# Kernel optimization log

Hardware: AMD Instinct MI355X
Metric: run time of the kernel (lower is better)

## Reference

```python
import jax, jax.numpy as jnp
import numpy as np

SENSORS = 50000
X_DIM = 64
HID = 64
Y_DIM = 32
N_EDGES = 800000


def setup_inputs() -> dict:
    key = jax.random.key(0)
    k0, k1, k2, k3 = jax.random.split(key, 4)
    x_input = jax.random.normal(k0, (1, X_DIM, SENSORS), dtype=jnp.float32)
    edge_index = jax.random.randint(k1, (2, N_EDGES), 0, SENSORS, dtype=jnp.int32)
    # GCNConv parameters (glorot-ish scaling)
    W1 = jax.random.normal(k2, (X_DIM, HID), dtype=jnp.float32) / np.sqrt(X_DIM)
    b1 = jnp.zeros((HID,), dtype=jnp.float32)
    W2 = jax.random.normal(k3, (HID, Y_DIM), dtype=jnp.float32) / np.sqrt(HID)
    b2 = jnp.zeros((Y_DIM,), dtype=jnp.float32)
    return {"x_input": x_input, "W1": W1, "b1": b1, "W2": W2, "b2": b2,
            "edge_index": edge_index}


def _gcn_conv(x, W, b, src, dst, n_nodes):
    """PyG GCNConv: x' = D^{-1/2}(A+I)D^{-1/2} (x W) + b."""
    h = x @ W  # [N, F_out]
    loop = jnp.arange(n_nodes, dtype=src.dtype)
    s = jnp.concatenate([src, loop])  # add self-loops
    d = jnp.concatenate([dst, loop])
    deg = jax.ops.segment_sum(jnp.ones_like(d, dtype=h.dtype), d,
                              num_segments=n_nodes)
    dinv = jnp.where(deg > 0, jax.lax.rsqrt(deg), 0.0)
    norm = dinv[s] * dinv[d]  # [E+N]
    msg = h[s] * norm[:, None]  # gather source features, scale
    out = jax.ops.segment_sum(msg, d, num_segments=n_nodes)  # scatter-add to targets
    return out + b


def reference(x_input, W1, b1, W2, b2, edge_index):
    B = x_input.shape[0]
    # [B, x, S] -> [B, S, x] -> [B*S, x]
    h = jnp.transpose(x_input, (0, 2, 1)).reshape(-1, X_DIM)
    n_nodes = h.shape[0]
    src, dst = edge_index[0], edge_index[1]
    h = _gcn_conv(h, W1, b1, src, dst, n_nodes)
    h = jax.nn.relu(h)
    h = _gcn_conv(h, W2, b2, src, dst, n_nodes)
    # [B*S, y] -> [B, S, y] -> [B, y, S]
    return jnp.transpose(h.reshape(B, SENSORS, Y_DIM), (0, 2, 1))
```

## Files before the change

### kernel.cpp

```cpp
#include <hip/hip_runtime.h>

#define NS 50000
#define NE 800000
#define XD 64
#define HD 64
#define YD 32

#define SHIFT 7
#define BNODES 128
#define NBUCK 391
#define BCAP 2560
#define NBLKA 256
#define EPB (NE / NBLKA)
#define SCAP 32
#define XW_BLKS ((NS + 255) / 256)

__device__ __forceinline__ unsigned f2b(float f) {
    union { float f; unsigned u; } c; c.f = f;
    return (c.u + 0x7fffu + ((c.u >> 16) & 1u)) >> 16;
}
__device__ __forceinline__ float blo(unsigned u) {
    union { unsigned u; float f; } c; c.u = u << 16; return c.f;
}
__device__ __forceinline__ float bhi(unsigned u) {
    union { unsigned u; float f; } c; c.u = u & 0xffff0000u; return c.f;
}

__global__ __launch_bounds__(256) void k_bktxw1(const int* __restrict__ src,
                                                const int* __restrict__ dst,
                                                int* __restrict__ cnt2,
                                                unsigned* __restrict__ ebuf2,
                                                const float* __restrict__ x,
                                                const float* __restrict__ W1,
                                                unsigned* __restrict__ G1h) {
    __shared__ unsigned se[EPB];
    __shared__ unsigned short lp[EPB];
    __shared__ int hist[NBUCK];
    __shared__ float w1f[XD * HD];
    int t = threadIdx.x;
    if (blockIdx.x < NBLKA) {
        int blk = blockIdx.x;
        int lo = blk * EPB;
        for (int i = t; i < NBUCK; i += 256) hist[i] = 0;
        __syncthreads();
        for (int i = t; i < EPB; i += 256) {
            unsigned d = (unsigned)__builtin_nontemporal_load(dst + lo + i);
            unsigned s = (unsigned)__builtin_nontemporal_load(src + lo + i);
            se[i] = (d << 16) | s;
            lp[i] = (unsigned short)atomicAdd(&hist[d >> SHIFT], 1);
        }
        __syncthreads();
        for (int i = t; i < NBUCK; i += 256)
            cnt2[blk * NBUCK + i] = min(hist[i], SCAP);
        for (int i = t; i < EPB; i += 256) {
            unsigned p = se[i];
            int b = p >> (16 + SHIFT);
            int pos = lp[i];
            if (pos < SCAP)
                ebuf2[((size_t)b * NBLKA + blk) * SCAP + pos] = p;
        }
        return;
    }
    for (int i = t; i < XD * HD; i += 256) w1f[i] = W1[i];
    __syncthreads();
    int node = (blockIdx.x - NBLKA) * 256 + t;
    if (node >= NS) return;
    float4 acc[16];
#pragma unroll
    for (int i = 0; i < 16; ++i) acc[i] = make_float4(0.f, 0.f, 0.f, 0.f);
    for (int xf = 0; xf < XD; ++xf) {
        float xv = __builtin_nontemporal_load(&x[(size_t)xf * NS + node]);
        const float4* wr = (const float4*)&w1f[xf * HD];
#pragma unroll
        for (int i = 0; i < 16; ++i) {
            float4 wv = wr[i];
            acc[i].x += xv * wv.x; acc[i].y += xv * wv.y;
            acc[i].z += xv * wv.z; acc[i].w += xv * wv.w;
        }
    }
    unsigned pk[32];
#pragma unroll
    for (int i = 0; i < 16; ++i) {
        pk[2 * i]     = f2b(acc[i].x) | (f2b(acc[i].y) << 16);
        pk[2 * i + 1] = f2b(acc[i].z) | (f2b(acc[i].w) << 16);
    }
    uint4* o = (uint4*)&G1h[(size_t)node * 32];
#pragma unroll
    for (int i = 0; i < 8; ++i) o[i] = ((uint4*)pk)[i];
}

__global__ __launch_bounds__(256) void k_sort(const unsigned* __restrict__ ebuf2,
                                              const int* __restrict__ cnt2,
                                              unsigned short* __restrict__ csr,
                                              int* __restrict__ beg,
                                              int* __restrict__ endp,
                                              float* __restrict__ dinv,
                                              unsigned* __restrict__ G1h) {
    __shared__ unsigned se[BCAP];
    __shared__ unsigned short lcsr[BCAP];
    __shared__ int cnt[BNODES];
    __shared__ int offl[BNODES];
    __shared__ int cur[BNODES];
    __shared__ int sm[256];
    __shared__ int wsum[4];
    int b = blockIdx.x, t = threadIdx.x;
    int lane = t & 63, w = t >> 6;
    int c = cnt2[t * NBUCK + b];
    int v = c;
#pragma unroll
    for (int d = 1; d < 64; d <<= 1) {
        int o = __shfl_up(v, d);
        if (lane >= d) v += o;
    }
    if (lane == 63) wsum[w] = v;
    if (t < BNODES) cnt[t] = 0;
    __syncthreads();
    int wpre = 0;
#pragma unroll
    for (int i = 0; i < 4; ++i) wpre += (i < w) ? wsum[i] : 0;
    int soff = wpre + v - c;
    int ntot = wsum[0] + wsum[1] + wsum[2] + wsum[3];
    int n = min(ntot, BCAP);
    {
        const unsigned* sb = ebuf2 + ((size_t)b * NBLKA + t) * SCAP;
        for (int j = 0; j < c; j += 4) {
            uint4 vv = *(const uint4*)&sb[j];
            int p = soff + j;
            if (p < BCAP) se[p] = vv.x;
            if (j + 1 < c && p + 1 < BCAP) se[p + 1] = vv.y;
            if (j + 2 < c && p + 2 < BCAP) se[p + 2] = vv.z;
            if (j + 3 < c && p + 3 < BCAP) se[p + 3] = vv.w;
        }
    }
    __syncthreads();
    for (int i = t; i < n; i += 256) atomicAdd(&cnt[(se[i] >> 16) & (BNODES - 1)], 1);
    __syncthreads();
    int v2 = (t < BNODES) ? cnt[t] : 0;
    sm[t] = v2;
    __syncthreads();
    int val2 = v2;
    for (int o = 1; o < BNODES; o <<= 1) {
        int other = (t >= o) ? sm[t - o] : 0;
        __syncthreads();
        val2 += other;
        sm[t] = val2;
        __syncthreads();
    }
    if (t < BNODES) { offl[t] = val2 - v2; cur[t] = val2 - v2; }
    __syncthreads();
    for (int i = t; i < n; i += 256) {
        unsigned p = se[i];
        int l = (p >> 16) & (BNODES - 1);
        int pos = atomicAdd(&cur[l], 1);
        lcsr[pos] = (unsigned short)(p & 0xffffu);
    }
    __syncthreads();
    unsigned* gc = (unsigned*)(csr + (size_t)b * BCAP);
    int nw = (n + 1) >> 1;
    for (int i = t; i < nw; i += 256) gc[i] = ((const unsigned*)lcsr)[i];
    if (t < BNODES) {
        int node = b * BNODES + t;
        if (node < NS) {
            int bg = b * BCAP + offl[t];
            beg[node] = bg;
            endp[node] = bg + cnt[t];
            dinv[node] = rsqrtf((float)cnt[t] + 1.0f);
        }
    }
    int tn = t >> 1, hf = t & 1;
    int node = b * BNODES + tn;
    if (node >= NS) return;
    float dv = rsqrtf((float)cnt[tn] + 1.0f);
    uint4* row = (uint4*)&G1h[(size_t)node * 32 + hf * 16];
#pragma unroll
    for (int i = 0; i < 4; ++i) {
        uint4 u = row[i];
        u.x = f2b(dv * blo(u.x)) | (f2b(dv * bhi(u.x)) << 16);
        u.y = f2b(dv * blo(u.y)) | (f2b(dv * bhi(u.y)) << 16);
        u.z = f2b(dv * blo(u.z)) | (f2b(dv * bhi(u.z)) << 16);
        u.w = f2b(dv * blo(u.w)) | (f2b(dv * bhi(u.w)) << 16);
        row[i] = u;
    }
}

__global__ __launch_bounds__(256) void k_g1l2(const int* __restrict__ beg,
                                              const int* __restrict__ endp,
                                              const unsigned short* __restrict__ csr,
                                              const unsigned* __restrict__ G1h,
                                              const float* __restrict__ dinv,
                                              const float* __restrict__ b1,
                                              const float* __restrict__ W2,
                                              unsigned* __restrict__ G2h) {
    __shared__ float w2s[HD * YD];
    __shared__ float bsh[HD];
    __shared__ float lds_h[16][68];
    __shared__ float lds_dv[16];
    int t = threadIdx.x;
    for (int i = t; i < HD * YD; i += 256) w2s[i] = W2[i];
    if (t < HD) bsh[t] = b1[t];
    __syncthreads();

    int nl = t >> 4;
    int l  = t & 15;
    int node = blockIdx.x * 16 + nl;
    int beg_ = beg[node], end_ = endp[node];
    float a0 = 0.f, a1 = 0.f, a2 = 0.f, a3 = 0.f;
#pragma unroll 4
    for (int e = beg_; e < end_; ++e) {
        int s = (int)csr[e];
        uint2 u = *(const uint2*)&G1h[(unsigned)s * 32u + 2u * l];
        a0 += blo(u.x); a1 += bhi(u.x);
        a2 += blo(u.y); a3 += bhi(u.y);
    }
    uint2 us = *(const uint2*)&G1h[(unsigned)node * 32u + 2u * l];
    float dv = dinv[node];
    float4 h;
    h.x = fmaxf(fmaf(dv, a0 + blo(us.x), bsh[4 * l + 0]), 0.f);
    h.y = fmaxf(fmaf(dv, a1 + bhi(us.x), bsh[4 * l + 1]), 0.f);
    h.z = fmaxf(fmaf(dv, a2 + blo(us.y), bsh[4 * l + 2]), 0.f);
    h.w = fmaxf(fmaf(dv, a3 + bhi(us.y), bsh[4 * l + 3]), 0.f);
    *(float4*)&lds_h[nl][4 * l] = h;
    if (l == 0) lds_dv[nl] = dv;
    __syncthreads();

    int n2 = t >> 4;
    int oo = (t & 15) * 2;
    float dv2 = lds_dv[n2];
    const float* hr = &lds_h[n2][0];
    float p0 = 0.f, p1 = 0.f;
#pragma unroll
    for (int f4 = 0; f4 < 16; ++f4) {
        float4 hv = *(const float4*)&hr[f4 * 4];
        float2 wa = *(const float2*)&w2s[(f4 * 4 + 0) * YD + oo];
        float2 wb = *(const float2*)&w2s[(f4 * 4 + 1) * YD + oo];
        float2 wc = *(const float2*)&w2s[(f4 * 4 + 2) * YD + oo];
        float2 wd = *(const float2*)&w2s[(f4 * 4 + 3) * YD + oo];
        p0 = fmaf(hv.x, wa.x, p0); p1 = fmaf(hv.x, wa.y, p1);
        p0 = fmaf(hv.y, wb.x, p0); p1 = fmaf(hv.y, wb.y, p1);
        p0 = fmaf(hv.z, wc.x, p0); p1 = fmaf(hv.z, wc.y, p1);
        p0 = fmaf(hv.w, wd.x, p0); p1 = fmaf(hv.w, wd.y, p1);
    }
    int node2 = blockIdx.x * 16 + n2;
    G2h[(size_t)node2 * 16 + (t & 15)] = f2b(dv2 * p0) | (f2b(dv2 * p1) << 16);
}

__global__ __launch_bounds__(256) void k_g2out(const int* __restrict__ beg,
                                               const int* __restrict__ endp,
                                               const unsigned short* __restrict__ csr,
                                               const unsigned* __restrict__ G2h,
                                               const float* __restrict__ dinv,
                                               const float* __restrict__ b2,
                                               float* __restrict__ out) {
    __shared__ float ot[32][33];
    __shared__ float b2s[YD];
    int t = threadIdx.x;
    if (t < YD) b2s[t] = b2[t];
    int g = t >> 3;
    int l = t & 7;
    int base_n = blockIdx.x * 32;
    int node = base_n + g;
    if (node < NS) {
        int beg_ = beg[node], end_ = endp[node];
        float a0 = 0.f, a1 = 0.f, a2 = 0.f, a3 = 0.f;
#pragma unroll 4
        for (int e = beg_; e < end_; ++e) {
            int s = (int)csr[e];
            uint2 u = *(const uint2*)&G2h[(unsigned)s * 16u + 2u * l];
            a0 += blo(u.x); a1 += bhi(u.x);
            a2 += blo(u.y); a3 += bhi(u.y);
        }
        uint2 us = *(const uint2*)&G2h[(unsigned)node * 16u + 2u * l];
        float dv = dinv[node];
        ot[g][4 * l + 0] = dv * (a0 + blo(us.x));
        ot[g][4 * l + 1] = dv * (a1 + bhi(us.x));
        ot[g][4 * l + 2] = dv * (a2 + blo(us.y));
        ot[g][4 * l + 3] = dv * (a3 + bhi(us.y));
    }
    __syncthreads();
#pragma unroll
    for (int k = 0; k < 4; ++k) {
        int idx = k * 256 + t;
        int o = idx >> 5, n = idx & 31;
        int nd = base_n + n;
        if (nd < NS)
            out[(size_t)o * NS + nd] = ot[n][o] + b2s[o];
    }
}

extern "C" void kernel_launch(void* const* d_in, const int* in_sizes, int n_in,
                              void* d_out, int out_size, void* d_ws, size_t ws_size,
                              hipStream_t stream) {
    const float* x  = (const float*)d_in[0];
    const float* W1 = (const float*)d_in[1];
    const float* b1 = (const float*)d_in[2];
    const float* W2 = (const float*)d_in[3];
    const float* b2 = (const float*)d_in[4];
    const int* ei   = (const int*)d_in[5];
    const int* src = ei;
    const int* dst = ei + NE;

    int* cnt2      = (int*)d_ws;
    unsigned* ebuf2 = (unsigned*)(cnt2 + NBLKA * NBUCK);
    unsigned short* csr = (unsigned short*)(ebuf2 + (size_t)NBUCK * NBLKA * SCAP);
    int* beg      = (int*)((unsigned*)csr + (size_t)NBUCK * BCAP / 2);
    int* endp     = beg + 50000;
    float* dinv   = (float*)(endp + 50000);
    unsigned* G1h = (unsigned*)(dinv + 50000);
    unsigned* G2h = G1h + (size_t)50000 * 32;
    float* out    = (float*)d_out;

    k_bktxw1<<<NBLKA + XW_BLKS, 256, 0, stream>>>(src, dst, cnt2, ebuf2, x, W1, G1h);
    k_sort<<<NBUCK, 256, 0, stream>>>(ebuf2, cnt2, csr, beg, endp, dinv, G1h);
    k_g1l2<<<NS / 16, 256, 0, stream>>>(beg, endp, csr, G1h, dinv, b1, W2, G2h);
    k_g2out<<<(NS + 31) / 32, 256, 0, stream>>>(beg, endp, csr, G2h, dinv, b2, out);
}
```

Measured before the change: 90.79 us.

## Apply source degree scaling in the gather instead of pre-scaling G1 rows

Drops the read-modify-write pass in the sort kernel that scaled every XW1 row by dinv. The layer-1 gather now loads dinv[s] per edge and fuses the scale into an FMA, with the self-loop term scaled by dv squared. The bucket/xw1 kernel's shared buffers are also unioned into one array, which lowers LDS use per block and may raise occupancy. The cost is an extra random 4-byte dinv load per edge in the gather loop, in exchange for removing a full pass over the 6.4MB G1 buffer and one bf16 rounding.

```diff
diff --git a/kernel.cpp b/kernel.cpp
--- a/kernel.cpp
+++ b/kernel.cpp
@@ -14,6 +14,7 @@
 #define EPB (NE / NBLKA)
 #define SCAP 32
 #define XW_BLKS ((NS + 255) / 256)
+#define SMEM_BYTES 20352
 
 __device__ __forceinline__ unsigned f2b(float f) {
     union { float f; unsigned u; } c; c.f = f;
@@ -32,13 +33,13 @@
                                                 unsigned* __restrict__ ebuf2,
                                                 const float* __restrict__ x,
                                                 const float* __restrict__ W1,
-                                                unsigned* __restrict__ G1h) {
-    __shared__ unsigned se[EPB];
-    __shared__ unsigned short lp[EPB];
-    __shared__ int hist[NBUCK];
-    __shared__ float w1f[XD * HD];
+                                                unsigned* __restrict__ U1h) {
+    __shared__ __align__(16) unsigned char smem[SMEM_BYTES];
     int t = threadIdx.x;
     if (blockIdx.x < NBLKA) {
+        unsigned* se = (unsigned*)smem;
+        unsigned short* lp = (unsigned short*)(smem + 12512);
+        int* hist = (int*)(smem + 18768);
         int blk = blockIdx.x;
         int lo = blk * EPB;
         for (int i = t; i < NBUCK; i += 256) hist[i] = 0;
@@ -61,6 +62,7 @@
         }
         return;
     }
+    float* w1f = (float*)smem;
     for (int i = t; i < XD * HD; i += 256) w1f[i] = W1[i];
     __syncthreads();
     int node = (blockIdx.x - NBLKA) * 256 + t;
@@ -84,7 +86,7 @@
         pk[2 * i]     = f2b(acc[i].x) | (f2b(acc[i].y) << 16);
         pk[2 * i + 1] = f2b(acc[i].z) | (f2b(acc[i].w) << 16);
     }
-    uint4* o = (uint4*)&G1h[(size_t)node * 32];
+    uint4* o = (uint4*)&U1h[(size_t)node * 32];
 #pragma unroll
     for (int i = 0; i < 8; ++i) o[i] = ((uint4*)pk)[i];
 }
@@ -94,8 +96,7 @@
                                               unsigned short* __restrict__ csr,
                                               int* __restrict__ beg,
                                               int* __restrict__ endp,
-                                              float* __restrict__ dinv,
-                                              unsigned* __restrict__ G1h) {
+                                              float* __restrict__ dinv) {
     __shared__ unsigned se[BCAP];
     __shared__ unsigned short lcsr[BCAP];
     __shared__ int cnt[BNODES];
@@ -167,26 +168,12 @@
             dinv[node] = rsqrtf((float)cnt[t] + 1.0f);
         }
     }
-    int tn = t >> 1, hf = t & 1;
-    int node = b * BNODES + tn;
-    if (node >= NS) return;
-    float dv = rsqrtf((float)cnt[tn] + 1.0f);
-    uint4* row = (uint4*)&G1h[(size_t)node * 32 + hf * 16];
-#pragma unroll
-    for (int i = 0; i < 4; ++i) {
-        uint4 u = row[i];
-        u.x = f2b(dv * blo(u.x)) | (f2b(dv * bhi(u.x)) << 16);
-        u.y = f2b(dv * blo(u.y)) | (f2b(dv * bhi(u.y)) << 16);
-        u.z = f2b(dv * blo(u.z)) | (f2b(dv * bhi(u.z)) << 16);
-        u.w = f2b(dv * blo(u.w)) | (f2b(dv * bhi(u.w)) << 16);
-        row[i] = u;
-    }
 }
 
 __global__ __launch_bounds__(256) void k_g1l2(const int* __restrict__ beg,
                                               const int* __restrict__ endp,
                                               const unsigned short* __restrict__ csr,
-                                              const unsigned* __restrict__ G1h,
+                                              const unsigned* __restrict__ U1h,
                                               const float* __restrict__ dinv,
                                               const float* __restrict__ b1,
                                               const float* __restrict__ W2,
@@ -208,17 +195,18 @@
 #pragma unroll 4
     for (int e = beg_; e < end_; ++e) {
         int s = (int)csr[e];
-        uint2 u = *(const uint2*)&G1h[(unsigned)s * 32u + 2u * l];
-        a0 += blo(u.x); a1 += bhi(u.x);
-        a2 += blo(u.y); a3 += bhi(u.y);
-    }
-    uint2 us = *(const uint2*)&G1h[(unsigned)node * 32u + 2u * l];
+        float dvs = dinv[s];
+        uint2 u = *(const uint2*)&U1h[(unsigned)s * 32u + 2u * l];
+        a0 = fmaf(dvs, blo(u.x), a0); a1 = fmaf(dvs, bhi(u.x), a1);
+        a2 = fmaf(dvs, blo(u.y), a2); a3 = fmaf(dvs, bhi(u.y), a3);
+    }
+    uint2 us = *(const uint2*)&U1h[(unsigned)node * 32u + 2u * l];
     float dv = dinv[node];
     float4 h;
-    h.x = fmaxf(fmaf(dv, a0 + blo(us.x), bsh[4 * l + 0]), 0.f);
-    h.y = fmaxf(fmaf(dv, a1 + bhi(us.x), bsh[4 * l + 1]), 0.f);
-    h.z = fmaxf(fmaf(dv, a2 + blo(us.y), bsh[4 * l + 2]), 0.f);
-    h.w = fmaxf(fmaf(dv, a3 + bhi(us.y), bsh[4 * l + 3]), 0.f);
+    h.x = fmaxf(fmaf(dv, fmaf(dv, blo(us.x), a0), bsh[4 * l + 0]), 0.f);
+    h.y = fmaxf(fmaf(dv, fmaf(dv, bhi(us.x), a1), bsh[4 * l + 1]), 0.f);
+    h.z = fmaxf(fmaf(dv, fmaf(dv, blo(us.y), a2), bsh[4 * l + 2]), 0.f);
+    h.w = fmaxf(fmaf(dv, fmaf(dv, bhi(us.y), a3), bsh[4 * l + 3]), 0.f);
     *(float4*)&lds_h[nl][4 * l] = h;
     if (l == 0) lds_dv[nl] = dv;
     __syncthreads();
@@ -305,12 +293,12 @@
     int* beg      = (int*)((unsigned*)csr + (size_t)NBUCK * BCAP / 2);
     int* endp     = beg + 50000;
     float* dinv   = (float*)(endp + 50000);
-    unsigned* G1h = (unsigned*)(dinv + 50000);
-    unsigned* G2h = G1h + (size_t)50000 * 32;
+    unsigned* U1h = (unsigned*)(dinv + 50000);
+    unsigned* G2h = U1h + (size_t)50000 * 32;
     float* out    = (float*)d_out;
 
-    k_bktxw1<<<NBLKA + XW_BLKS, 256, 0, stream>>>(src, dst, cnt2, ebuf2, x, W1, G1h);
-    k_sort<<<NBUCK, 256, 0, stream>>>(ebuf2, cnt2, csr, beg, endp, dinv, G1h);
-    k_g1l2<<<NS / 16, 256, 0, stream>>>(beg, endp, csr, G1h, dinv, b1, W2, G2h);
+    k_bktxw1<<<NBLKA + XW_BLKS, 256, 0, stream>>>(src, dst, cnt2, ebuf2, x, W1, U1h);
+    k_sort<<<NBUCK, 256, 0, stream>>>(ebuf2, cnt2, csr, beg, endp, dinv);
+    k_g1l2<<<NS / 16, 256, 0, stream>>>(beg, endp, csr, U1h, dinv, b1, W2, G2h);
     k_g2out<<<(NS + 31) / 32, 256, 0, stream>>>(beg, endp, csr, G2h, dinv, b2, out);
 }
```

Result: faster. 88.86 us (-2.1%).
